# Kernel optimization log

Measured on AMD Instinct MI355X. Metric: run time of the kernel, lower is better.

Reference implementation:

```python
import jax, jax.numpy as jnp
import numpy as np

N = 100000        # nodes
E_HALF = 800000   # random edges before symmetrization
HID = 128         # hidden_dim
K = 4             # Chebyshev order
NEG = 0.01        # leaky_relu negative slope
BN_EPS = 1e-5
L2_EPS = 1e-12


def setup_inputs() -> dict:
    key = jax.random.key(0)
    ks = jax.random.split(key, 4)
    x = jax.random.normal(ks[0], (N, 3), dtype=jnp.float32)
    e = jax.random.randint(ks[1], (2, E_HALF), 0, N, dtype=jnp.int32)
    # symmetrize so the sym-normalized Laplacian is well defined
    edge_index = jnp.concatenate([e, e[::-1]], axis=1).astype(jnp.int64)

    def wcheb(k, fin, fout):
        return jax.random.normal(k, (K, fin, fout), dtype=jnp.float32) * np.float32(1.0 / np.sqrt(fin * K))

    wk = jax.random.split(ks[2], 5)
    return {
        "x": x, "edge_index": edge_index,
        "W1": wcheb(wk[0], 3, HID),   "b1": jnp.zeros((HID,), jnp.float32),
        "W2": wcheb(wk[1], HID, HID), "b2": jnp.zeros((HID,), jnp.float32),
        "W3": wcheb(wk[2], HID, HID), "b3": jnp.zeros((HID,), jnp.float32),
        "W4": wcheb(wk[3], HID, HID), "b4": jnp.zeros((HID,), jnp.float32),
        "g1": jnp.ones((HID,), jnp.float32), "be1": jnp.zeros((HID,), jnp.float32),
        "g2": jnp.ones((HID,), jnp.float32), "be2": jnp.zeros((HID,), jnp.float32),
        "g3": jnp.ones((HID,), jnp.float32), "be3": jnp.zeros((HID,), jnp.float32),
        "Wrep": jax.random.normal(wk[4], (HID, 3), dtype=jnp.float32) * np.float32(1.0 / np.sqrt(HID)),
        "brep": jnp.zeros((3,), jnp.float32),
    }


def _cheb(x, src, dst, norm, W, b):
    """PyG ChebConv (sym norm, lambda_max=2): out = sum_k T_k(L_hat) x @ W_k + b."""
    def prop(t):  # (L_hat t)_i = sum_{e: src->dst==i} norm_e * t[src_e]
        return jax.ops.segment_sum(t[src] * norm[:, None], dst, num_segments=N)
    Tx0 = x
    out = Tx0 @ W[0]
    Tx1 = prop(Tx0)
    out = out + Tx1 @ W[1]
    for k in range(2, W.shape[0]):
        Tx2 = 2.0 * prop(Tx1) - Tx0
        out = out + Tx2 @ W[k]
        Tx0, Tx1 = Tx1, Tx2
    return out + b


def _bn(x, g, b):  # BatchNorm1d, training mode (batch stats, biased var)
    mu = x.mean(axis=0)
    var = ((x - mu) ** 2).mean(axis=0)
    return (x - mu) * jax.lax.rsqrt(var + BN_EPS) * g + b


def _leaky(x):
    return jnp.where(x >= 0, x, NEG * x)


def reference(x, edge_index, W1, b1, W2, b2, W3, b3, W4, b4,
              g1, be1, g2, be2, g3, be3, Wrep, brep):
    src, dst = edge_index[0], edge_index[1]
    deg = jax.ops.segment_sum(jnp.ones(src.shape, jnp.float32), src, num_segments=N)
    dinv = jnp.where(deg > 0, jax.lax.rsqrt(jnp.maximum(deg, 1.0)), 0.0)
    # scaled Laplacian L_hat = -D^{-1/2} A D^{-1/2} (zero diagonal) for lambda_max=2
    norm = -(dinv[src] * dinv[dst])  # [E]

    h = _cheb(x.astype(jnp.float32), src, dst, norm, W1, b1)
    h = _bn(_leaky(h), g1, be1)
    h = _cheb(h, src, dst, norm, W2, b2)
    h = _bn(_leaky(h), g2, be2)
    h = _cheb(h, src, dst, norm, W3, b3)
    h = _bn(jnp.maximum(h, 0.0), g3, be3)
    h = _cheb(h, src, dst, norm, W4, b4)
    h = h / jnp.maximum(jnp.linalg.norm(h, axis=1, keepdims=True), L2_EPS)
    return h @ Wrep + brep  # [N, 3]
```

## Files before the change

### kernel.cpp

```cpp
#include <hip/hip_runtime.h>
#include <hip/hip_bf16.h>


#define HID 128
#define NEG 0.01f
#define BN_EPS 1e-5f
#define L2_EPS 1e-12f
#define CAP 64

typedef __attribute__((ext_vector_type(8))) short short8;
typedef __attribute__((ext_vector_type(4))) float floatx4;

__device__ __forceinline__ short f2bf(float f) {
    unsigned u = __float_as_uint(f);
    return (short)((u + 0x7fffu + ((u >> 16) & 1u)) >> 16);
}
__device__ __forceinline__ unsigned pack2bf(float x, float y) {
    return (unsigned)(unsigned short)f2bf(x) | ((unsigned)(unsigned short)f2bf(y) << 16);
}
__device__ __forceinline__ float bflo(unsigned u) { return __uint_as_float(u << 16); }
__device__ __forceinline__ float bfhi(unsigned u) { return __uint_as_float(u & 0xffff0000u); }
__device__ __forceinline__ float bf2f(unsigned short h) { return __uint_as_float((unsigned)h << 16); }

__device__ __forceinline__ float actf(float v, int act) {
    if (act == 0) return v >= 0.f ? v : NEG * v;
    if (act == 1) return v > 0.f ? v : 0.f;
    return v;
}


__global__ __launch_bounds__(256) void k_zero(int* __restrict__ arr, float* __restrict__ S, int N) {
    int i = blockIdx.x * 256 + threadIdx.x;
    if (i < N) arr[i * CAP] = 0;
    if (blockIdx.x == 0) {
        for (int k = threadIdx.x; k < 1024; k += 256) S[k] = 0.f;
    }
}

__global__ __launch_bounds__(256) void k_fillpad(const int* __restrict__ src, const int* __restrict__ dst,
                                                 int* __restrict__ arr, int E) {
    int e = blockIdx.x * 256 + threadIdx.x;
    if (e >= E) return;
    int d = dst[e];
    int pos = atomicAdd(&arr[d * CAP], 1);
    if (pos < CAP - 1) arr[d * CAP + 1 + pos] = src[e];
}

__global__ __launch_bounds__(256) void k_dinv(const int* __restrict__ arr, float* __restrict__ dinv,
                                              int* __restrict__ cnt, int N) {
    int i = blockIdx.x * 256 + threadIdx.x;
    if (i < N) {
        int d = arr[i * CAP];
        dinv[i] = d > 0 ? rsqrtf((float)d) : 0.f;
        cnt[i] = d < CAP - 1 ? d : CAP - 1;
    }
}

__global__ __launch_bounds__(256) void k_norm(const int* __restrict__ arr, const int* __restrict__ cnt,
                                              const float* __restrict__ dinv, int2* __restrict__ edges,
                                              int N) {
    int node = blockIdx.x * 4 + (threadIdx.x >> 6);
    if (node >= N) return;
    node = __builtin_amdgcn_readfirstlane(node);
    int lane = threadIdx.x & 63;
    int deg = cnt[node];
    float dd = dinv[node];
    if (lane < deg) {
        int s = arr[node * CAP + 1 + lane];
        int2 rec;
        rec.x = s;
        rec.y = __float_as_int(-(dinv[s] * dd));
        edges[node * CAP + lane] = rec;
    }
}


__global__ __launch_bounds__(256) void k_prop3(const float* __restrict__ T, const float* __restrict__ prev,
                                               float* __restrict__ out, const int* __restrict__ cnt,
                                               const int2* __restrict__ edges,
                                               float a, float b, int N) {
    int i = blockIdx.x * 256 + threadIdx.x;
    if (i >= N) return;
    float a0 = 0.f, a1 = 0.f, a2 = 0.f;
    int deg = cnt[i];
    int base = i * CAP;
    for (int j = 0; j < deg; ++j) {
        int2 r = edges[base + j];
        float w = __int_as_float(r.y);
        a0 += w * T[r.x * 3 + 0];
        a1 += w * T[r.x * 3 + 1];
        a2 += w * T[r.x * 3 + 2];
    }
    float r0 = a * a0, r1 = a * a1, r2 = a * a2;
    if (prev) {
        r0 += b * prev[i * 3 + 0];
        r1 += b * prev[i * 3 + 1];
        r2 += b * prev[i * 3 + 2];
    }
    out[i * 3 + 0] = r0;
    out[i * 3 + 1] = r1;
    out[i * 3 + 2] = r2;
}

__global__ __launch_bounds__(256) void k_prop128(const unsigned* __restrict__ T, const unsigned* __restrict__ prev,
                                                 unsigned* __restrict__ out, const int* __restrict__ cnt,
                                                 const int2* __restrict__ edges,
                                                 float a, float b, int N) {
    int node = blockIdx.x * 4 + (threadIdx.x >> 6);
    if (node >= N) return;
    node = __builtin_amdgcn_readfirstlane(node);
    int lane = threadIdx.x & 63;
    int deg = cnt[node];
    const int2* eb = edges + (size_t)node * CAP;
    float accx = 0.f, accy = 0.f;
    int j = 0;
    int nb = deg >> 3;
    if (nb > 0) {
        int2 recA[8]; unsigned tA[8];
        int2 recB[8]; unsigned tB[8];
        #pragma unroll
        for (int k = 0; k < 8; ++k) recA[k] = eb[k];
        #pragma unroll
        for (int k = 0; k < 8; ++k) tA[k] = T[(size_t)recA[k].x * 64 + lane];
        for (int bi = 1; bi < nb; ++bi) {
            const int2* ebb = eb + bi * 8;
            #pragma unroll
            for (int k = 0; k < 8; ++k) recB[k] = ebb[k];
            #pragma unroll
            for (int k = 0; k < 8; ++k) tB[k] = T[(size_t)recB[k].x * 64 + lane];
            #pragma unroll
            for (int k = 0; k < 8; ++k) {
                float w = __int_as_float(recA[k].y);
                accx += w * bflo(tA[k]);
                accy += w * bfhi(tA[k]);
            }
            #pragma unroll
            for (int k = 0; k < 8; ++k) { recA[k] = recB[k]; tA[k] = tB[k]; }
        }
        #pragma unroll
        for (int k = 0; k < 8; ++k) {
            float w = __int_as_float(recA[k].y);
            accx += w * bflo(tA[k]);
            accy += w * bfhi(tA[k]);
        }
        j = nb * 8;
    }
    for (; j < deg; ++j) {
        int2 r = eb[j];
        float w = __int_as_float(r.y);
        unsigned t0 = T[(size_t)r.x * 64 + lane];
        accx += w * bflo(t0);
        accy += w * bfhi(t0);
    }
    float rx = a * accx, ry = a * accy;
    if (prev) {
        unsigned p = __builtin_nontemporal_load(&prev[(size_t)node * 64 + lane]);
        rx += b * bflo(p);
        ry += b * bfhi(p);
    }
    __builtin_nontemporal_store(pack2bf(rx, ry), &out[(size_t)node * 64 + lane]);
}


__global__ __launch_bounds__(256) void k_gemm1(const float* __restrict__ x, const float* __restrict__ t1,
                                               const float* __restrict__ t2, const float* __restrict__ t3,
                                               const float* __restrict__ W, const float* __restrict__ b,
                                               unsigned short* __restrict__ OUT, int N) {
    __shared__ float Wl[12 * 128];
    __shared__ float bl[128];
    int tid = threadIdx.x;
    for (int i = tid; i < 1536; i += 256) Wl[i] = W[i];
    if (tid < 128) bl[tid] = b[tid];
    __syncthreads();
    int node = blockIdx.x * 2 + (tid >> 7);
    if (node >= N) return;
    int f = tid & 127;
    float acc = bl[f];
    const float* rows[4] = {x, t1, t2, t3};
    #pragma unroll
    for (int k = 0; k < 4; ++k) {
        const float* r = rows[k] + (size_t)node * 3;
        acc += r[0] * Wl[(k * 3 + 0) * 128 + f];
        acc += r[1] * Wl[(k * 3 + 1) * 128 + f];
        acc += r[2] * Wl[(k * 3 + 2) * 128 + f];
    }
    OUT[(size_t)node * 128 + f] = (unsigned short)f2bf(acc);
}


__global__ __launch_bounds__(256) void k_packW(const float* __restrict__ WA, const float* __restrict__ WB,
                                               const float* __restrict__ WC, short* __restrict__ Wp) {
    int gid = blockIdx.x * 256 + threadIdx.x;
    int L = gid >> 16;
    int idx = gid & 65535;
    int j = idx & 7;
    int lane = (idx >> 3) & 63;
    int rest = idx >> 9;
    int nt = rest & 7;
    int ks = rest >> 3;
    int kk = ks * 32 + (lane >> 4) * 8 + j;
    int c = nt * 16 + (lane & 15);
    const float* W = (L == 0) ? WA : (L == 1) ? WB : WC;
    Wp[gid] = f2bf(W[(size_t)(kk >> 7) * 16384 + (kk & 127) * 128 + c]);
}

__global__ __launch_bounds__(512) void k_gemm512(const short* __restrict__ T0, const short* __restrict__ T1,
                                                 const short* __restrict__ T2, const short* __restrict__ T3,
                                                 const short* __restrict__ Wp, const float* __restrict__ bias,
                                                 unsigned short* __restrict__ OUT, float* __restrict__ S,
                                                 int M, int doStats, int act) {
    __shared__ short Wlds[65536];
    __shared__ float sS[256];
    int tid = threadIdx.x;
    int lane = tid & 63, wave = tid >> 6;
    if (tid < 256) sS[tid] = 0.f;
    for (int i = tid; i < 8192; i += 512) ((int4*)Wlds)[i] = ((const int4*)Wp)[i];
    __syncthreads();

    int quad = lane >> 4;
    int col0 = lane & 15;
    const short* Ts[4] = {T0, T1, T2, T3};
    float s1[8], s2[8];
    #pragma unroll
    for (int i = 0; i < 8; ++i) { s1[i] = 0.f; s2[i] = 0.f; }

    int nt32 = (M + 31) / 32;
    int stride = gridDim.x * 8;
    for (int t = blockIdx.x * 8 + wave; t < nt32; t += stride) {
        int r0 = t * 32;
        int rowa = r0 + col0;
        int rowb = rowa + 16;
        size_t rb0 = (size_t)(rowa < M ? rowa : M - 1) * 128;
        size_t rb1 = (size_t)(rowb < M ? rowb : M - 1) * 128;
        floatx4 acc0[8], acc1[8];
        #pragma unroll
        for (int i = 0; i < 8; ++i) {
            acc0[i][0] = 0.f; acc0[i][1] = 0.f; acc0[i][2] = 0.f; acc0[i][3] = 0.f;
            acc1[i][0] = 0.f; acc1[i][1] = 0.f; acc1[i][2] = 0.f; acc1[i][3] = 0.f;
        }
        #pragma unroll 4
        for (int ks = 0; ks < 16; ++ks) {
            const short* Tm = Ts[ks >> 2];
            int aoff = (ks & 3) * 32 + quad * 8;
            short8 af0 = *((const short8*)(Tm + rb0 + aoff));
            short8 af1 = *((const short8*)(Tm + rb1 + aoff));
            #pragma unroll
            for (int nt = 0; nt < 8; ++nt) {
                short8 bf = *((const short8*)(Wlds + ((ks * 8 + nt) * 64 + lane) * 8));
                acc0[nt] = __builtin_amdgcn_mfma_f32_16x16x32_bf16(af0, bf, acc0[nt], 0, 0, 0);
                acc1[nt] = __builtin_amdgcn_mfma_f32_16x16x32_bf16(af1, bf, acc1[nt], 0, 0, 0);
            }
        }
        #pragma unroll
        for (int half = 0; half < 2; ++half) {
            int rbase = r0 + half * 16 + quad * 4;
            #pragma unroll
            for (int nt = 0; nt < 8; ++nt) {
                int c = nt * 16 + col0;
                float bv = bias[c];
                #pragma unroll
                for (int rg = 0; rg < 4; ++rg) {
                    int r = rbase + rg;
                    if (r < M) {
                        float v = (half ? acc1[nt][rg] : acc0[nt][rg]) + bv;
                        unsigned short h = (unsigned short)f2bf(v);
                        OUT[(size_t)r * 128 + c] = h;
                        float u = actf(bf2f(h), act);
                        s1[nt] += u;
                        s2[nt] += u * u;
                    }
                }
            }
        }
    }
    if (doStats) {
        #pragma unroll
        for (int nt = 0; nt < 8; ++nt) {
            int c = nt * 16 + col0;
            atomicAdd(&sS[c], s1[nt]);
            atomicAdd(&sS[c + 128], s2[nt]);
        }
        __syncthreads();
        if (tid < 256) atomicAdd(&S[tid], sS[tid]);
    }
}


__global__ __launch_bounds__(256) void k_stats(const unsigned* __restrict__ X, float* __restrict__ S,
                                               int N, int act) {
    int u = threadIdx.x & 63, rh = threadIdx.x >> 6;
    int r0 = blockIdx.x * 512;
    int rend = r0 + 512 < N ? r0 + 512 : N;
    float s1x = 0.f, s2x = 0.f, s1y = 0.f, s2y = 0.f;
    for (int r = r0 + rh; r < rend; r += 4) {
        unsigned v = X[(size_t)r * 64 + u];
        float a = actf(bflo(v), act), b = actf(bfhi(v), act);
        s1x += a; s2x += a * a;
        s1y += b; s2y += b * b;
    }
    int c = 2 * u;
    atomicAdd(&S[c], s1x);
    atomicAdd(&S[c + 1], s1y);
    atomicAdd(&S[c + 128], s2x);
    atomicAdd(&S[c + 129], s2y);
}

__global__ __launch_bounds__(256) void k_bnapply(const unsigned* __restrict__ X, const float* __restrict__ S,
                                                 const float* __restrict__ g, const float* __restrict__ be,
                                                 unsigned* __restrict__ Y, int n4, int act, float invN) {
    int i = blockIdx.x * 256 + threadIdx.x;
    if (i >= n4) return;
    uint2 v = ((const uint2*)X)[i];
    int col = (i * 4) & 127;
    float4 m1 = *((const float4*)(S + col));
    float4 m2 = *((const float4*)(S + 128 + col));
    float4 gg = *((const float4*)(g + col));
    float4 bb = *((const float4*)(be + col));
    float mu, var, aa, cc;
    float vx, vy, vz, vw;
    mu = m1.x * invN; var = m2.x * invN - mu * mu; aa = gg.x * rsqrtf(var + BN_EPS); cc = bb.x - mu * aa;
    vx = actf(bflo(v.x), act) * aa + cc;
    mu = m1.y * invN; var = m2.y * invN - mu * mu; aa = gg.y * rsqrtf(var + BN_EPS); cc = bb.y - mu * aa;
    vy = actf(bfhi(v.x), act) * aa + cc;
    mu = m1.z * invN; var = m2.z * invN - mu * mu; aa = gg.z * rsqrtf(var + BN_EPS); cc = bb.z - mu * aa;
    vz = actf(bflo(v.y), act) * aa + cc;
    mu = m1.w * invN; var = m2.w * invN - mu * mu; aa = gg.w * rsqrtf(var + BN_EPS); cc = bb.w - mu * aa;
    vw = actf(bfhi(v.y), act) * aa + cc;
    uint2 o;
    o.x = pack2bf(vx, vy);
    o.y = pack2bf(vz, vw);
    ((uint2*)Y)[i] = o;
}


__global__ __launch_bounds__(256) void k_final(const unsigned* __restrict__ H, const float* __restrict__ Wrep,
                                               const float* __restrict__ brep, float* __restrict__ out, int N) {
    int node = blockIdx.x * 4 + (threadIdx.x >> 6);
    if (node >= N) return;
    int lane = threadIdx.x & 63;
    unsigned u = H[(size_t)node * 64 + lane];
    float hx = bflo(u), hy = bfhi(u);
    int f0 = 2 * lane;
    float nrm = hx * hx + hy * hy;
    float p0 = hx * Wrep[f0 * 3 + 0] + hy * Wrep[(f0 + 1) * 3 + 0];
    float p1 = hx * Wrep[f0 * 3 + 1] + hy * Wrep[(f0 + 1) * 3 + 1];
    float p2 = hx * Wrep[f0 * 3 + 2] + hy * Wrep[(f0 + 1) * 3 + 2];
    #pragma unroll
    for (int d = 1; d < 64; d <<= 1) {
        nrm += __shfl_xor(nrm, d);
        p0 += __shfl_xor(p0, d);
        p1 += __shfl_xor(p1, d);
        p2 += __shfl_xor(p2, d);
    }
    if (lane == 0) {
        float inv = 1.f / fmaxf(sqrtf(nrm), L2_EPS);
        out[node * 3 + 0] = p0 * inv + brep[0];
        out[node * 3 + 1] = p1 * inv + brep[1];
        out[node * 3 + 2] = p2 * inv + brep[2];
    }
}


extern "C" void kernel_launch(void* const* d_in, const int* in_sizes, int n_in,
                              void* d_out, int out_size, void* d_ws, size_t ws_size,
                              hipStream_t stream) {
    const int N = in_sizes[0] / 3;
    const int E = in_sizes[1] / 2;

    const float* x    = (const float*)d_in[0];
    const int*   ei   = (const int*)d_in[1];
    const int* esrc = ei;
    const int* edst = ei + E;
    const float* W1 = (const float*)d_in[2];  const float* b1 = (const float*)d_in[3];
    const float* W2 = (const float*)d_in[4];  const float* b2 = (const float*)d_in[5];
    const float* W3 = (const float*)d_in[6];  const float* b3 = (const float*)d_in[7];
    const float* W4 = (const float*)d_in[8];  const float* b4 = (const float*)d_in[9];
    const float* g1 = (const float*)d_in[10]; const float* be1 = (const float*)d_in[11];
    const float* g2 = (const float*)d_in[12]; const float* be2 = (const float*)d_in[13];
    const float* g3 = (const float*)d_in[14]; const float* be3 = (const float*)d_in[15];
    const float* Wrep = (const float*)d_in[16]; const float* brep = (const float*)d_in[17];
    float* out = (float*)d_out;

    char* w = (char*)d_ws;
    size_t off = 0;
    auto alloc = [&](size_t bytes) { size_t o = off; off = (off + bytes + 255) & ~(size_t)255; return o; };
    int*   arr    = (int*)(w + alloc((size_t)N * CAP * 4));
    int*   cnt    = (int*)(w + alloc((size_t)N * 4));
    float* dinv   = (float*)(w + alloc((size_t)N * 4));
    int2*  edges  = (int2*)(w + alloc((size_t)N * CAP * 8));
    short* Wp     = (short*)(w + alloc(3 * 65536 * 2));
    float* S      = (float*)(w + alloc(4 * 256 * 4));
    float* t1f    = (float*)(w + alloc((size_t)N * 3 * 4));
    float* t2f    = (float*)(w + alloc((size_t)N * 3 * 4));
    float* t3f    = (float*)(w + alloc((size_t)N * 3 * 4));
    short* T0     = (short*)(w + alloc((size_t)N * 128 * 2));
    short* T1     = (short*)(w + alloc((size_t)N * 128 * 2));
    short* T2     = (short*)(w + alloc((size_t)N * 128 * 2));
    short* T3     = (short*)(w + alloc((size_t)N * 128 * 2));
    unsigned short* OUT = (unsigned short*)(w + alloc((size_t)N * 128 * 2));

    int gE = (E + 255) / 256;
    int gN = (N + 255) / 256;
    int gW = (N + 3) / 4;
    float invN = 1.f / (float)N;

    k_zero<<<gN, 256, 0, stream>>>(arr, S, N);
    k_fillpad<<<gE, 256, 0, stream>>>(esrc, edst, arr, E);
    k_dinv<<<gN, 256, 0, stream>>>(arr, dinv, cnt, N);
    k_norm<<<gW, 256, 0, stream>>>(arr, cnt, dinv, edges, N);
    k_packW<<<768, 256, 0, stream>>>(W2, W3, W4, Wp);

    k_prop3<<<gN, 256, 0, stream>>>(x, nullptr, t1f, cnt, edges, 1.f, 0.f, N);
    k_prop3<<<gN, 256, 0, stream>>>(t1f, x, t2f, cnt, edges, 2.f, -1.f, N);
    k_prop3<<<gN, 256, 0, stream>>>(t2f, t1f, t3f, cnt, edges, 2.f, -1.f, N);
    k_gemm1<<<(N + 1) / 2, 256, 0, stream>>>(x, t1f, t2f, t3f, W1, b1, OUT, N);
    k_stats<<<(N + 511) / 512, 256, 0, stream>>>((const unsigned*)OUT, S, N, 0);
    k_bnapply<<<(N * 32 + 255) / 256, 256, 0, stream>>>((const unsigned*)OUT, S, g1, be1,
                                                        (unsigned*)T0, N * 32, 0, invN);

    const float* bs[3]  = {b2, b3, b4};
    const float* gs[3]  = {g2, g3, nullptr};
    const float* bes[3] = {be2, be3, nullptr};
    int acts[3] = {0, 1, 2};

    for (int l = 0; l < 3; ++l) {
        const unsigned* U0 = (const unsigned*)T0;
        unsigned* U1 = (unsigned*)T1;
        unsigned* U2 = (unsigned*)T2;
        unsigned* U3 = (unsigned*)T3;
        k_prop128<<<gW, 256, 0, stream>>>(U0, nullptr, U1, cnt, edges, 1.f, 0.f, N);
        k_prop128<<<gW, 256, 0, stream>>>((const unsigned*)U1, U0, U2, cnt, edges, 2.f, -1.f, N);
        k_prop128<<<gW, 256, 0, stream>>>((const unsigned*)U2, (const unsigned*)U1, U3, cnt, edges, 2.f, -1.f, N);
        float* Sl = S + (size_t)(l + 1) * 256;
        k_gemm512<<<256, 512, 0, stream>>>(T0, T1, T2, T3, Wp + (size_t)l * 65536, bs[l], OUT, Sl, N,
                                           l < 2 ? 1 : 0, acts[l]);
        if (l < 2) {
            k_bnapply<<<(N * 32 + 255) / 256, 256, 0, stream>>>((const unsigned*)OUT, Sl, gs[l], bes[l],
                                                                (unsigned*)T0, N * 32, acts[l], invN);
        }
    }

    k_final<<<gW, 256, 0, stream>>>((const unsigned*)OUT, Wrep, brep, out, N);
}
```

Before: 1.152 ms.

## Fuse BatchNorm apply into first propagation, stats into gemm1, final head into gemm

Removes the separate stats, BN-apply and final kernels. The BN affine transform is applied on the fly inside the first propagation of each layer, using the linearity of the Laplacian and a per-node row sum of the norm weights (snorm) to fold the shift term. The same kernel also writes T0. gemm1 now accumulates BN statistics with a persistent-block loop. The last gemm computes the L2 norm and the 3-wide projection directly from its accumulators. This saves several full passes over the N×128 activations, in exchange for recomputing the activation per gathered neighbour and a somewhat different rounding order.

```diff
diff --git a/kernel.cpp b/kernel.cpp
--- a/kernel.cpp
+++ b/kernel.cpp
@@ -58,20 +58,25 @@
 
 __global__ __launch_bounds__(256) void k_norm(const int* __restrict__ arr, const int* __restrict__ cnt,
                                               const float* __restrict__ dinv, int2* __restrict__ edges,
-                                              int N) {
+                                              float* __restrict__ snorm, int N) {
     int node = blockIdx.x * 4 + (threadIdx.x >> 6);
     if (node >= N) return;
     node = __builtin_amdgcn_readfirstlane(node);
     int lane = threadIdx.x & 63;
     int deg = cnt[node];
     float dd = dinv[node];
+    int s = (lane < deg) ? arr[node * CAP + 1 + lane] : 0;
+    float w = (lane < deg) ? -(dinv[s] * dd) : 0.f;
     if (lane < deg) {
-        int s = arr[node * CAP + 1 + lane];
         int2 rec;
         rec.x = s;
-        rec.y = __float_as_int(-(dinv[s] * dd));
+        rec.y = __float_as_int(w);
         edges[node * CAP + lane] = rec;
     }
+    float sw = w;
+    #pragma unroll
+    for (int d = 1; d < 64; d <<= 1) sw += __shfl_xor(sw, d);
+    if (lane == 0) snorm[node] = sw;
 }
 
 
@@ -100,6 +105,74 @@
     out[i * 3 + 0] = r0;
     out[i * 3 + 1] = r1;
     out[i * 3 + 2] = r2;
+}
+
+__global__ __launch_bounds__(256) void k_prop1(const unsigned* __restrict__ OUT,
+                                               unsigned* __restrict__ T1, unsigned* __restrict__ T0,
+                                               const int* __restrict__ cnt, const int2* __restrict__ edges,
+                                               const float* __restrict__ snorm, const float* __restrict__ S,
+                                               const float* __restrict__ g, const float* __restrict__ be,
+                                               int act, float invN, int N) {
+    int node = blockIdx.x * 4 + (threadIdx.x >> 6);
+    if (node >= N) return;
+    node = __builtin_amdgcn_readfirstlane(node);
+    int lane = threadIdx.x & 63;
+    int f0 = 2 * lane;
+    float mu0 = S[f0] * invN, mu1 = S[f0 + 1] * invN;
+    float v0 = S[f0 + 128] * invN - mu0 * mu0;
+    float v1 = S[f0 + 129] * invN - mu1 * mu1;
+    float a0 = g[f0] * rsqrtf(v0 + BN_EPS), a1 = g[f0 + 1] * rsqrtf(v1 + BN_EPS);
+    float c0 = be[f0] - mu0 * a0, c1 = be[f0 + 1] - mu1 * a1;
+
+    int deg = cnt[node];
+    const int2* eb = edges + (size_t)node * CAP;
+    float accx = 0.f, accy = 0.f;
+    int j = 0;
+    int nb = deg >> 3;
+    if (nb > 0) {
+        int2 recA[8]; unsigned tA[8];
+        int2 recB[8]; unsigned tB[8];
+        #pragma unroll
+        for (int k = 0; k < 8; ++k) recA[k] = eb[k];
+        #pragma unroll
+        for (int k = 0; k < 8; ++k) tA[k] = OUT[(size_t)recA[k].x * 64 + lane];
+        for (int bi = 1; bi < nb; ++bi) {
+            const int2* ebb = eb + bi * 8;
+            #pragma unroll
+            for (int k = 0; k < 8; ++k) recB[k] = ebb[k];
+            #pragma unroll
+            for (int k = 0; k < 8; ++k) tB[k] = OUT[(size_t)recB[k].x * 64 + lane];
+            #pragma unroll
+            for (int k = 0; k < 8; ++k) {
+                float w = __int_as_float(recA[k].y);
+                accx += w * actf(bflo(tA[k]), act);
+                accy += w * actf(bfhi(tA[k]), act);
+            }
+            #pragma unroll
+            for (int k = 0; k < 8; ++k) { recA[k] = recB[k]; tA[k] = tB[k]; }
+        }
+        #pragma unroll
+        for (int k = 0; k < 8; ++k) {
+            float w = __int_as_float(recA[k].y);
+            accx += w * actf(bflo(tA[k]), act);
+            accy += w * actf(bfhi(tA[k]), act);
+        }
+        j = nb * 8;
+    }
+    for (; j < deg; ++j) {
+        int2 r = eb[j];
+        float w = __int_as_float(r.y);
+        unsigned t0 = OUT[(size_t)r.x * 64 + lane];
+        accx += w * actf(bflo(t0), act);
+        accy += w * actf(bfhi(t0), act);
+    }
+    float si = snorm[node];
+    __builtin_nontemporal_store(pack2bf(a0 * accx + si * c0, a1 * accy + si * c1),
+                                &T1[(size_t)node * 64 + lane]);
+    unsigned h = OUT[(size_t)node * 64 + lane];
+    float t0lo = a0 * actf(bflo(h), act) + c0;
+    float t0hi = a1 * actf(bfhi(h), act) + c1;
+    __builtin_nontemporal_store(pack2bf(t0lo, t0hi), &T0[(size_t)node * 64 + lane]);
 }
 
 __global__ __launch_bounds__(256) void k_prop128(const unsigned* __restrict__ T, const unsigned* __restrict__ prev,
@@ -165,26 +238,40 @@
 __global__ __launch_bounds__(256) void k_gemm1(const float* __restrict__ x, const float* __restrict__ t1,
                                                const float* __restrict__ t2, const float* __restrict__ t3,
                                                const float* __restrict__ W, const float* __restrict__ b,
-                                               unsigned short* __restrict__ OUT, int N) {
+                                               unsigned short* __restrict__ OUT, float* __restrict__ S,
+                                               int npb, int N) {
     __shared__ float Wl[12 * 128];
     __shared__ float bl[128];
+    __shared__ float sS[256];
     int tid = threadIdx.x;
     for (int i = tid; i < 1536; i += 256) Wl[i] = W[i];
     if (tid < 128) bl[tid] = b[tid];
+    if (tid < 256) sS[tid] = 0.f;
     __syncthreads();
-    int node = blockIdx.x * 2 + (tid >> 7);
-    if (node >= N) return;
     int f = tid & 127;
-    float acc = bl[f];
+    int base = blockIdx.x * npb;
+    int end = base + npb < N ? base + npb : N;
     const float* rows[4] = {x, t1, t2, t3};
-    #pragma unroll
-    for (int k = 0; k < 4; ++k) {
-        const float* r = rows[k] + (size_t)node * 3;
-        acc += r[0] * Wl[(k * 3 + 0) * 128 + f];
-        acc += r[1] * Wl[(k * 3 + 1) * 128 + f];
-        acc += r[2] * Wl[(k * 3 + 2) * 128 + f];
-    }
-    OUT[(size_t)node * 128 + f] = (unsigned short)f2bf(acc);
+    float s1 = 0.f, s2 = 0.f;
+    for (int node = base + (tid >> 7); node < end; node += 2) {
+        float acc = bl[f];
+        #pragma unroll
+        for (int k = 0; k < 4; ++k) {
+            const float* r = rows[k] + (size_t)node * 3;
+            acc += r[0] * Wl[(k * 3 + 0) * 128 + f];
+            acc += r[1] * Wl[(k * 3 + 1) * 128 + f];
+            acc += r[2] * Wl[(k * 3 + 2) * 128 + f];
+        }
+        unsigned short h = (unsigned short)f2bf(acc);
+        OUT[(size_t)node * 128 + f] = h;
+        float u = actf(bf2f(h), 0);
+        s1 += u;
+        s2 += u * u;
+    }
+    atomicAdd(&sS[f], s1);
+    atomicAdd(&sS[f + 128], s2);
+    __syncthreads();
+    if (tid < 256) atomicAdd(&S[tid], sS[tid]);
 }
 
 
@@ -208,12 +295,19 @@
                                                  const short* __restrict__ T2, const short* __restrict__ T3,
                                                  const short* __restrict__ Wp, const float* __restrict__ bias,
                                                  unsigned short* __restrict__ OUT, float* __restrict__ S,
-                                                 int M, int doStats, int act) {
+                                                 const float* __restrict__ Wrep, const float* __restrict__ brep,
+                                                 float* __restrict__ fout,
+                                                 int M, int doStats, int doFinal, int act) {
     __shared__ short Wlds[65536];
     __shared__ float sS[256];
+    __shared__ float sW[388];
     int tid = threadIdx.x;
     int lane = tid & 63, wave = tid >> 6;
     if (tid < 256) sS[tid] = 0.f;
+    if (doFinal) {
+        for (int i = tid; i < 384; i += 512) sW[i] = Wrep[i];
+        if (tid < 3) sW[384 + tid] = brep[tid];
+    }
     for (int i = tid; i < 8192; i += 512) ((int4*)Wlds)[i] = ((const int4*)Wp)[i];
     __syncthreads();
 
@@ -251,23 +345,56 @@
                 acc1[nt] = __builtin_amdgcn_mfma_f32_16x16x32_bf16(af1, bf, acc1[nt], 0, 0, 0);
             }
         }
-        #pragma unroll
-        for (int half = 0; half < 2; ++half) {
-            int rbase = r0 + half * 16 + quad * 4;
-            #pragma unroll
-            for (int nt = 0; nt < 8; ++nt) {
-                int c = nt * 16 + col0;
-                float bv = bias[c];
+        if (doFinal) {
+            #pragma unroll
+            for (int half = 0; half < 2; ++half) {
                 #pragma unroll
                 for (int rg = 0; rg < 4; ++rg) {
-                    int r = rbase + rg;
-                    if (r < M) {
-                        float v = (half ? acc1[nt][rg] : acc0[nt][rg]) + bv;
-                        unsigned short h = (unsigned short)f2bf(v);
-                        OUT[(size_t)r * 128 + c] = h;
-                        float u = actf(bf2f(h), act);
-                        s1[nt] += u;
-                        s2[nt] += u * u;
+                    int r = r0 + half * 16 + quad * 4 + rg;
+                    float sq = 0.f, p0 = 0.f, p1 = 0.f, p2 = 0.f;
+                    #pragma unroll
+                    for (int nt = 0; nt < 8; ++nt) {
+                        int c = nt * 16 + col0;
+                        float v = (half ? acc1[nt][rg] : acc0[nt][rg]) + bias[c];
+                        sq += v * v;
+                        p0 += v * sW[c * 3 + 0];
+                        p1 += v * sW[c * 3 + 1];
+                        p2 += v * sW[c * 3 + 2];
+                    }
+                    #pragma unroll
+                    for (int d = 1; d < 16; d <<= 1) {
+                        sq += __shfl_xor(sq, d);
+                        p0 += __shfl_xor(p0, d);
+                        p1 += __shfl_xor(p1, d);
+                        p2 += __shfl_xor(p2, d);
+                    }
+                    if (col0 == 0 && r < M) {
+                        float inv = 1.f / fmaxf(sqrtf(sq), L2_EPS);
+                        fout[r * 3 + 0] = p0 * inv + sW[384];
+                        fout[r * 3 + 1] = p1 * inv + sW[385];
+                        fout[r * 3 + 2] = p2 * inv + sW[386];
+                    }
+                }
+            }
+        } else {
+            #pragma unroll
+            for (int half = 0; half < 2; ++half) {
+                int rbase = r0 + half * 16 + quad * 4;
+                #pragma unroll
+                for (int nt = 0; nt < 8; ++nt) {
+                    int c = nt * 16 + col0;
+                    float bv = bias[c];
+                    #pragma unroll
+                    for (int rg = 0; rg < 4; ++rg) {
+                        int r = rbase + rg;
+                        if (r < M) {
+                            float v = (half ? acc1[nt][rg] : acc0[nt][rg]) + bv;
+                            unsigned short h = (unsigned short)f2bf(v);
+                            OUT[(size_t)r * 128 + c] = h;
+                            float u = actf(bf2f(h), act);
+                            s1[nt] += u;
+                            s2[nt] += u * u;
+                        }
                     }
                 }
             }
@@ -282,81 +409,6 @@
         }
         __syncthreads();
         if (tid < 256) atomicAdd(&S[tid], sS[tid]);
-    }
-}
-
-
-__global__ __launch_bounds__(256) void k_stats(const unsigned* __restrict__ X, float* __restrict__ S,
-                                               int N, int act) {
-    int u = threadIdx.x & 63, rh = threadIdx.x >> 6;
-    int r0 = blockIdx.x * 512;
-    int rend = r0 + 512 < N ? r0 + 512 : N;
-    float s1x = 0.f, s2x = 0.f, s1y = 0.f, s2y = 0.f;
-    for (int r = r0 + rh; r < rend; r += 4) {
-        unsigned v = X[(size_t)r * 64 + u];
-        float a = actf(bflo(v), act), b = actf(bfhi(v), act);
-        s1x += a; s2x += a * a;
-        s1y += b; s2y += b * b;
-    }
-    int c = 2 * u;
-    atomicAdd(&S[c], s1x);
-    atomicAdd(&S[c + 1], s1y);
-    atomicAdd(&S[c + 128], s2x);
-    atomicAdd(&S[c + 129], s2y);
-}
-
-__global__ __launch_bounds__(256) void k_bnapply(const unsigned* __restrict__ X, const float* __restrict__ S,
-                                                 const float* __restrict__ g, const float* __restrict__ be,
-                                                 unsigned* __restrict__ Y, int n4, int act, float invN) {
-    int i = blockIdx.x * 256 + threadIdx.x;
-    if (i >= n4) return;
-    uint2 v = ((const uint2*)X)[i];
-    int col = (i * 4) & 127;
-    float4 m1 = *((const float4*)(S + col));
-    float4 m2 = *((const float4*)(S + 128 + col));
-    float4 gg = *((const float4*)(g + col));
-    float4 bb = *((const float4*)(be + col));
-    float mu, var, aa, cc;
-    float vx, vy, vz, vw;
-    mu = m1.x * invN; var = m2.x * invN - mu * mu; aa = gg.x * rsqrtf(var + BN_EPS); cc = bb.x - mu * aa;
-    vx = actf(bflo(v.x), act) * aa + cc;
-    mu = m1.y * invN; var = m2.y * invN - mu * mu; aa = gg.y * rsqrtf(var + BN_EPS); cc = bb.y - mu * aa;
-    vy = actf(bfhi(v.x), act) * aa + cc;
-    mu = m1.z * invN; var = m2.z * invN - mu * mu; aa = gg.z * rsqrtf(var + BN_EPS); cc = bb.z - mu * aa;
-    vz = actf(bflo(v.y), act) * aa + cc;
-    mu = m1.w * invN; var = m2.w * invN - mu * mu; aa = gg.w * rsqrtf(var + BN_EPS); cc = bb.w - mu * aa;
-    vw = actf(bfhi(v.y), act) * aa + cc;
-    uint2 o;
-    o.x = pack2bf(vx, vy);
-    o.y = pack2bf(vz, vw);
-    ((uint2*)Y)[i] = o;
-}
-
-
-__global__ __launch_bounds__(256) void k_final(const unsigned* __restrict__ H, const float* __restrict__ Wrep,
-                                               const float* __restrict__ brep, float* __restrict__ out, int N) {
-    int node = blockIdx.x * 4 + (threadIdx.x >> 6);
-    if (node >= N) return;
-    int lane = threadIdx.x & 63;
-    unsigned u = H[(size_t)node * 64 + lane];
-    float hx = bflo(u), hy = bfhi(u);
-    int f0 = 2 * lane;
-    float nrm = hx * hx + hy * hy;
-    float p0 = hx * Wrep[f0 * 3 + 0] + hy * Wrep[(f0 + 1) * 3 + 0];
-    float p1 = hx * Wrep[f0 * 3 + 1] + hy * Wrep[(f0 + 1) * 3 + 1];
-    float p2 = hx * Wrep[f0 * 3 + 2] + hy * Wrep[(f0 + 1) * 3 + 2];
-    #pragma unroll
-    for (int d = 1; d < 64; d <<= 1) {
-        nrm += __shfl_xor(nrm, d);
-        p0 += __shfl_xor(p0, d);
-        p1 += __shfl_xor(p1, d);
-        p2 += __shfl_xor(p2, d);
-    }
-    if (lane == 0) {
-        float inv = 1.f / fmaxf(sqrtf(nrm), L2_EPS);
-        out[node * 3 + 0] = p0 * inv + brep[0];
-        out[node * 3 + 1] = p1 * inv + brep[1];
-        out[node * 3 + 2] = p2 * inv + brep[2];
     }
 }
 
@@ -387,6 +439,7 @@
     int*   arr    = (int*)(w + alloc((size_t)N * CAP * 4));
     int*   cnt    = (int*)(w + alloc((size_t)N * 4));
     float* dinv   = (float*)(w + alloc((size_t)N * 4));
+    float* snorm  = (float*)(w + alloc((size_t)N * 4));
     int2*  edges  = (int2*)(w + alloc((size_t)N * CAP * 8));
     short* Wp     = (short*)(w + alloc(3 * 65536 * 2));
     float* S      = (float*)(w + alloc(4 * 256 * 4));
@@ -403,42 +456,38 @@
     int gN = (N + 255) / 256;
     int gW = (N + 3) / 4;
     float invN = 1.f / (float)N;
+    int npb = (N + 255) / 256;
 
     k_zero<<<gN, 256, 0, stream>>>(arr, S, N);
     k_fillpad<<<gE, 256, 0, stream>>>(esrc, edst, arr, E);
     k_dinv<<<gN, 256, 0, stream>>>(arr, dinv, cnt, N);
-    k_norm<<<gW, 256, 0, stream>>>(arr, cnt, dinv, edges, N);
+    k_norm<<<gW, 256, 0, stream>>>(arr, cnt, dinv, edges, snorm, N);
     k_packW<<<768, 256, 0, stream>>>(W2, W3, W4, Wp);
 
     k_prop3<<<gN, 256, 0, stream>>>(x, nullptr, t1f, cnt, edges, 1.f, 0.f, N);
     k_prop3<<<gN, 256, 0, stream>>>(t1f, x, t2f, cnt, edges, 2.f, -1.f, N);
     k_prop3<<<gN, 256, 0, stream>>>(t2f, t1f, t3f, cnt, edges, 2.f, -1.f, N);
-    k_gemm1<<<(N + 1) / 2, 256, 0, stream>>>(x, t1f, t2f, t3f, W1, b1, OUT, N);
-    k_stats<<<(N + 511) / 512, 256, 0, stream>>>((const unsigned*)OUT, S, N, 0);
-    k_bnapply<<<(N * 32 + 255) / 256, 256, 0, stream>>>((const unsigned*)OUT, S, g1, be1,
-                                                        (unsigned*)T0, N * 32, 0, invN);
+    k_gemm1<<<256, 256, 0, stream>>>(x, t1f, t2f, t3f, W1, b1, OUT, S, npb, N);
 
     const float* bs[3]  = {b2, b3, b4};
     const float* gs[3]  = {g2, g3, nullptr};
     const float* bes[3] = {be2, be3, nullptr};
-    int acts[3] = {0, 1, 2};
+    int actsIn[3] = {0, 0, 1};
+    int actsOut[3] = {0, 1, 2};
 
     for (int l = 0; l < 3; ++l) {
-        const unsigned* U0 = (const unsigned*)T0;
-        unsigned* U1 = (unsigned*)T1;
-        unsigned* U2 = (unsigned*)T2;
-        unsigned* U3 = (unsigned*)T3;
-        k_prop128<<<gW, 256, 0, stream>>>(U0, nullptr, U1, cnt, edges, 1.f, 0.f, N);
-        k_prop128<<<gW, 256, 0, stream>>>((const unsigned*)U1, U0, U2, cnt, edges, 2.f, -1.f, N);
-        k_prop128<<<gW, 256, 0, stream>>>((const unsigned*)U2, (const unsigned*)U1, U3, cnt, edges, 2.f, -1.f, N);
-        float* Sl = S + (size_t)(l + 1) * 256;
-        k_gemm512<<<256, 512, 0, stream>>>(T0, T1, T2, T3, Wp + (size_t)l * 65536, bs[l], OUT, Sl, N,
-                                           l < 2 ? 1 : 0, acts[l]);
-        if (l < 2) {
-            k_bnapply<<<(N * 32 + 255) / 256, 256, 0, stream>>>((const unsigned*)OUT, Sl, gs[l], bes[l],
-                                                                (unsigned*)T0, N * 32, acts[l], invN);
-        }
-    }
-
-    k_final<<<gW, 256, 0, stream>>>((const unsigned*)OUT, Wrep, brep, out, N);
-}
+        float* Sin = S + (size_t)l * 256;
+        float* Sout = S + (size_t)(l + 1) * 256;
+        const float* gc = (l == 0) ? g1 : gs[l - 1];
+        const float* bc = (l == 0) ? be1 : bes[l - 1];
+        k_prop1<<<gW, 256, 0, stream>>>((const unsigned*)OUT, (unsigned*)T1, (unsigned*)T0,
+                                        cnt, edges, snorm, Sin, gc, bc, actsIn[l], invN, N);
+        k_prop128<<<gW, 256, 0, stream>>>((const unsigned*)T1, (const unsigned*)T0, (unsigned*)T2,
+                                          cnt, edges, 2.f, -1.f, N);
+        k_prop128<<<gW, 256, 0, stream>>>((const unsigned*)T2, (const unsigned*)T1, (unsigned*)T3,
+                                          cnt, edges, 2.f, -1.f, N);
+        k_gemm512<<<256, 512, 0, stream>>>(T0, T1, T2, T3, Wp + (size_t)l * 65536, bs[l], OUT, Sout,
+                                           Wrep, brep, out, N,
+                                           l < 2 ? 1 : 0, l == 2 ? 1 : 0, actsOut[l]);
+    }
+}
```

After: 1.080 ms. 1.07x faster.
